# Optimization experiments

Hardware: AMD Instinct MI355X
Metric: run time of the kernel (lower is better)

Reference implementation:

```python
import jax, jax.numpy as jnp
import numpy as np

H = 256          # hidden_size
TH_X = 0.05      # delta threshold on inputs
TH_H = 0.05      # delta threshold on hidden state
F_IN = 6         # engineered feature count


def hardswish(v):
    return v * jnp.clip(v + 3.0, 0.0, 6.0) / 6.0


def setup_inputs() -> dict:
    key = jax.random.key(0)
    ks = jax.random.split(key, 6)
    B, T = 32, 4096
    x = jax.random.normal(ks[0], (B, T, 2), dtype=jnp.float32)
    # x2h: Linear(6, 3H, bias=False) -> weight (3H, 6)
    Wx = jax.random.normal(ks[1], (3 * H, F_IN), dtype=jnp.float32) * (1.0 / np.sqrt(F_IN))
    # h2h: Linear(H, 3H, bias=False) -> weight (3H, H)
    Wh = jax.random.normal(ks[2], (3 * H, H), dtype=jnp.float32) * (1.0 / np.sqrt(H))
    # fc_out: Linear(H, 2, bias=False)
    Wo = jax.random.normal(ks[3], (2, H), dtype=jnp.float32) * (1.0 / np.sqrt(H))
    # tcn conv1: Conv1d(2, 3, k=3, padding=16, dilation=16, bias=False) -> (O,I,K)=(3,2,3)
    Wc1 = jax.random.normal(ks[4], (3, 2, 3), dtype=jnp.float32) * 0.3
    # tcn conv2: Conv1d(3, 2, k=1) -> (2,3,1)
    Wc2 = jax.random.normal(ks[5], (2, 3, 1), dtype=jnp.float32) * 0.3
    return {"x": x, "Wx": Wx, "Wh": Wh, "Wo": Wo, "Wc1": Wc1, "Wc2": Wc2}


def _delta_gru(feats_TBF, Wx, Wh):
    # feats_TBF: (T, B, 6). Initial states are always zeros (the torch module
    # resets them whenever x_p_0 is None, which DeltaGRUModel always passes).
    T, B, F = feats_TBF.shape
    dt = feats_TBF.dtype
    carry0 = (
        jnp.zeros((B, F), dt),        # x_p
        jnp.zeros((B, H), dt),        # h
        jnp.zeros((B, H), dt),        # h_p
        jnp.zeros((B, H), dt),        # dm_nh
        jnp.zeros((B, 3 * H), dt),    # dm
    )

    def step(carry, xt):
        x_p, h, h_p, dm_nh, dm = carry
        dx = xt - x_p
        dh = h - h_p
        dxa = jnp.abs(dx)
        dha = jnp.abs(dh)
        dx = jnp.where(dxa < TH_X, 0.0, dx)
        dh = jnp.where(dha < TH_H, 0.0, dh)
        x_p = jnp.where(dxa >= TH_X, xt, x_p)
        h_p = jnp.where(dha >= TH_H, h, h_p)
        mac_x = dx @ Wx.T + dm          # (B, 3H)
        mac_h = dh @ Wh.T               # (B, 3H)
        mxr, mxz, mxn = jnp.split(mac_x, 3, axis=1)
        mhr, mhz, mhn = jnp.split(mac_h, 3, axis=1)
        dm_r = mxr + mhr
        dm_z = mxz + mhz
        dm_n = mxn
        dm_nh = mhn + dm_nh
        dm = jnp.concatenate([dm_r, dm_z, dm_n], axis=1)
        r = jax.nn.sigmoid(dm_r)
        z = jax.nn.sigmoid(dm_z)
        n = jnp.tanh(dm_n + r * dm_nh)
        h = (1.0 - z) * n + z * h
        return (x_p, h, h_p, dm_nh, dm), h

    _, hs = jax.lax.scan(step, carry0, feats_TBF)  # hs: (T, B, H)
    return hs


def reference(x, Wx, Wh, Wo, Wc1, Wc2):
    # x: (B, T, 2)
    B, T, _ = x.shape
    # --- TCN skip path ---
    xc = jnp.transpose(x, (0, 2, 1))  # (B, 2, T)
    c1 = jax.lax.conv_general_dilated(
        xc, Wc1, window_strides=(1,), padding=[(16, 16)], rhs_dilation=(16,),
        dimension_numbers=("NCH", "OIH", "NCH"))
    c2 = jax.lax.conv_general_dilated(
        hardswish(c1), Wc2, window_strides=(1,), padding=[(0, 0)],
        dimension_numbers=("NCH", "OIH", "NCH"))
    skip = jnp.transpose(hardswish(c2), (0, 2, 1))  # (B, T, 2)
    # --- engineered features ---
    i = x[..., 0:1]
    q = x[..., 1:2]
    amp2 = i * i + q * q
    amp = jnp.sqrt(jnp.maximum(amp2, 1e-12))
    amp3 = amp * amp2
    i_prev = jnp.pad(i[:, :-1, :], ((0, 0), (1, 0), (0, 0)))
    q_prev = jnp.pad(q[:, :-1, :], ((0, 0), (1, 0), (0, 0)))
    feats = jnp.concatenate([i, q, amp, amp3, i_prev, q_prev], axis=-1)  # (B,T,6)
    # --- delta-GRU scan (time-major) ---
    hs = _delta_gru(jnp.transpose(feats, (1, 0, 2)), Wx, Wh)  # (T, B, H)
    out = jnp.transpose(hs, (1, 0, 2))  # (B, T, H)
    return out @ Wo.T + skip  # (B, T, 2)
```

## Files before the change

### kernel.cpp

```cpp
#include <hip/hip_runtime.h>
#include <math.h>

#define HH 256
#define FIN 6
#define TT 4096
#define BB 32
#define TH 0.05f

typedef _Float16 h2 __attribute__((ext_vector_type(2)));
struct H8 { h2 a, b, c, d; };

__device__ __forceinline__ float hswish(float v) {
    float c = fminf(fmaxf(v + 3.0f, 0.0f), 6.0f);
    return v * c * (1.0f / 6.0f);
}
__device__ __forceinline__ float fexp2(float x) { return __builtin_amdgcn_exp2f(x); }
__device__ __forceinline__ float frcp(float x)  { return __builtin_amdgcn_rcpf(x); }
__device__ __forceinline__ float sigm(float x)  { return frcp(1.0f + fexp2(-1.44269504f * x)); }
__device__ __forceinline__ float tanhf_fast(float x) {
    float ax = fabsf(x);
    float e = fexp2(2.88539008f * ax);
    float t = 1.0f - 2.0f * frcp(e + 1.0f);
    return copysignf(t, x);
}

__device__ __forceinline__ float dpp_row_sum16(float p) {
    int x = __float_as_int(p);
    p += __int_as_float(__builtin_amdgcn_update_dpp(0, x, 0x118, 0xF, 0xF, true));
    x = __float_as_int(p);
    p += __int_as_float(__builtin_amdgcn_update_dpp(0, x, 0x114, 0xF, 0xF, true));
    x = __float_as_int(p);
    p += __int_as_float(__builtin_amdgcn_update_dpp(0, x, 0x112, 0xF, 0xF, true));
    x = __float_as_int(p);
    p += __int_as_float(__builtin_amdgcn_update_dpp(0, x, 0x111, 0xF, 0xF, true));
    return p;
}

__global__ __launch_bounds__(256) void k_prep(
        const float* __restrict__ x, const float* __restrict__ Wc1,
        const float* __restrict__ Wc2, float* __restrict__ feats,
        float* __restrict__ out) {
    int idx = blockIdx.x * 256 + threadIdx.x;
    if (idx >= BB * TT) return;
    int b = idx >> 12;
    int t = idx & (TT - 1);
    const float* xb = x + (size_t)b * TT * 2;
    float i0 = xb[t * 2 + 0], q0 = xb[t * 2 + 1];
    float ip = (t > 0) ? xb[(t - 1) * 2 + 0] : 0.0f;
    float qp = (t > 0) ? xb[(t - 1) * 2 + 1] : 0.0f;
    float amp2 = i0 * i0 + q0 * q0;
    float amp  = sqrtf(fmaxf(amp2, 1e-12f));
    float amp3 = amp * amp2;
    float* f = feats + (size_t)idx * 6;
    f[0] = i0; f[1] = q0; f[2] = amp; f[3] = amp3; f[4] = ip; f[5] = qp;

    float c1[3];
#pragma unroll
    for (int m = 0; m < 3; m++) {
        float acc = 0.0f;
#pragma unroll
        for (int k = 0; k < 3; k++) {
            int tt = t + (k - 1) * 16;
            if (tt >= 0 && tt < TT) {
                acc += Wc1[m * 6 + 0 * 3 + k] * xb[tt * 2 + 0];
                acc += Wc1[m * 6 + 1 * 3 + k] * xb[tt * 2 + 1];
            }
        }
        c1[m] = hswish(acc);
    }
#pragma unroll
    for (int o = 0; o < 2; o++) {
        float acc = Wc2[o * 3 + 0] * c1[0] + Wc2[o * 3 + 1] * c1[1] + Wc2[o * 3 + 2] * c1[2];
        out[(size_t)idx * 2 + o] = hswish(acc);
    }
}

__global__ __launch_bounds__(512)
__attribute__((amdgpu_waves_per_eu(2, 2))) void k_gru(
        const float* __restrict__ feats, const float* __restrict__ Wx,
        const float* __restrict__ Wh, const float* __restrict__ Wo,
        float* __restrict__ out) {
    __shared__ float s_out[TT * 2];
    __shared__ __align__(16) _Float16 s_dhh[2][HH];
    __shared__ __align__(16) float s_dx[2][8];
    __shared__ float s_feat[2][128 * FIN];

    const int tid  = threadIdx.x;
    const int wv   = tid >> 6;
    const int lane = tid & 63;
    const int half = lane >> 5;
    const int row  = wv * 32 + (lane & 31);
    const int b    = blockIdx.x;
    const float* fb = feats + (size_t)b * TT * FIN;

    for (int i = tid; i < TT * 2; i += 512) s_out[i] = 0.0f;
    for (int i = tid; i < 128 * FIN; i += 512) s_feat[0][i] = fb[i];

    h2 wr[64], wz[64], wn[64];
    {
        const int k0 = half * 128;
        const float4* p0 = (const float4*)(Wh + (size_t)(0 * HH + row) * HH + k0);
        const float4* p1 = (const float4*)(Wh + (size_t)(1 * HH + row) * HH + k0);
        const float4* p2 = (const float4*)(Wh + (size_t)(2 * HH + row) * HH + k0);
#pragma unroll
        for (int c = 0; c < 32; c++) {
            float4 v0 = p0[c], v1 = p1[c], v2 = p2[c];
            wr[2 * c]     = h2{(_Float16)v0.x, (_Float16)v0.y};
            wr[2 * c + 1] = h2{(_Float16)v0.z, (_Float16)v0.w};
            wz[2 * c]     = h2{(_Float16)v1.x, (_Float16)v1.y};
            wz[2 * c + 1] = h2{(_Float16)v1.z, (_Float16)v1.w};
            wn[2 * c]     = h2{(_Float16)v2.x, (_Float16)v2.y};
            wn[2 * c + 1] = h2{(_Float16)v2.z, (_Float16)v2.w};
        }
    }
    float wxr[FIN], wxz[FIN], wxn[FIN];
#pragma unroll
    for (int f = 0; f < FIN; f++) {
        wxr[f] = Wx[(size_t)(0 * HH + row) * FIN + f];
        wxz[f] = Wx[(size_t)(1 * HH + row) * FIN + f];
        wxn[f] = Wx[(size_t)(2 * HH + row) * FIN + f];
    }
    const float woc = Wo[half * HH + row];

    float h = 0.0f, hp = 0.0f, dmr = 0.0f, dmz = 0.0f, dmn = 0.0f, dmnh = 0.0f;
    float xp = 0.0f, curf = 0.0f;
    if (tid < FIN) curf = fb[tid];

    __syncthreads();

    for (int t = 0; t < TT; t++) {
        const int tb = t & 1;

        if ((t & 127) == 64 && t + 64 < TT) {
            const int w = (t >> 7) + 1;
            for (int i = tid; i < 128 * FIN; i += 512)
                s_feat[w & 1][i] = fb[(size_t)w * 128 * FIN + i];
        }

        {
            float dh = h - hp;
            bool keep = fabsf(dh) >= TH;
            if (half == 0) s_dhh[tb][row] = (_Float16)(keep ? dh : 0.0f);
            if (keep) hp = h;
        }
        if (tid < FIN) {
            float dx = curf - xp;
            bool keep = fabsf(dx) >= TH;
            s_dx[tb][tid] = keep ? dx : 0.0f;
            if (keep) xp = curf;
        }
        __syncthreads();

        float mxr = dmr, mxz = dmz, mxn = dmn;
        {
            const float4* dx4 = (const float4*)s_dx[tb];
            float4 da = dx4[0], db = dx4[1];
            mxr = fmaf(da.x, wxr[0], mxr); mxz = fmaf(da.x, wxz[0], mxz); mxn = fmaf(da.x, wxn[0], mxn);
            mxr = fmaf(da.y, wxr[1], mxr); mxz = fmaf(da.y, wxz[1], mxz); mxn = fmaf(da.y, wxn[1], mxn);
            mxr = fmaf(da.z, wxr[2], mxr); mxz = fmaf(da.z, wxz[2], mxz); mxn = fmaf(da.z, wxn[2], mxn);
            mxr = fmaf(da.w, wxr[3], mxr); mxz = fmaf(da.w, wxz[3], mxz); mxn = fmaf(da.w, wxn[3], mxn);
            mxr = fmaf(db.x, wxr[4], mxr); mxz = fmaf(db.x, wxz[4], mxz); mxn = fmaf(db.x, wxn[4], mxn);
            mxr = fmaf(db.y, wxr[5], mxr); mxz = fmaf(db.y, wxz[5], mxz); mxn = fmaf(db.y, wxn[5], mxn);
        }
        float ar0 = 0.0f, az0 = 0.0f, an0 = 0.0f;
        float ar1 = 0.0f, az1 = 0.0f, an1 = 0.0f;
        {
            const H8* dp = (const H8*)s_dhh[tb] + half * 16;
#pragma unroll
            for (int c = 0; c < 16; c += 2) {
                H8 d0 = dp[c];
                H8 d1 = dp[c + 1];
                ar0 = __builtin_amdgcn_fdot2(d0.a, wr[4 * c + 0], ar0, false);
                az0 = __builtin_amdgcn_fdot2(d0.a, wz[4 * c + 0], az0, false);
                an0 = __builtin_amdgcn_fdot2(d0.a, wn[4 * c + 0], an0, false);
                ar1 = __builtin_amdgcn_fdot2(d1.a, wr[4 * c + 4], ar1, false);
                az1 = __builtin_amdgcn_fdot2(d1.a, wz[4 * c + 4], az1, false);
                an1 = __builtin_amdgcn_fdot2(d1.a, wn[4 * c + 4], an1, false);
                ar0 = __builtin_amdgcn_fdot2(d0.b, wr[4 * c + 1], ar0, false);
                az0 = __builtin_amdgcn_fdot2(d0.b, wz[4 * c + 1], az0, false);
                an0 = __builtin_amdgcn_fdot2(d0.b, wn[4 * c + 1], an0, false);
                ar1 = __builtin_amdgcn_fdot2(d1.b, wr[4 * c + 5], ar1, false);
                az1 = __builtin_amdgcn_fdot2(d1.b, wz[4 * c + 5], az1, false);
                an1 = __builtin_amdgcn_fdot2(d1.b, wn[4 * c + 5], an1, false);
                ar0 = __builtin_amdgcn_fdot2(d0.c, wr[4 * c + 2], ar0, false);
                az0 = __builtin_amdgcn_fdot2(d0.c, wz[4 * c + 2], az0, false);
                an0 = __builtin_amdgcn_fdot2(d0.c, wn[4 * c + 2], an0, false);
                ar1 = __builtin_amdgcn_fdot2(d1.c, wr[4 * c + 6], ar1, false);
                az1 = __builtin_amdgcn_fdot2(d1.c, wz[4 * c + 6], az1, false);
                an1 = __builtin_amdgcn_fdot2(d1.c, wn[4 * c + 6], an1, false);
                ar0 = __builtin_amdgcn_fdot2(d0.d, wr[4 * c + 3], ar0, false);
                az0 = __builtin_amdgcn_fdot2(d0.d, wz[4 * c + 3], az0, false);
                an0 = __builtin_amdgcn_fdot2(d0.d, wn[4 * c + 3], an0, false);
                ar1 = __builtin_amdgcn_fdot2(d1.d, wr[4 * c + 7], ar1, false);
                az1 = __builtin_amdgcn_fdot2(d1.d, wz[4 * c + 7], az1, false);
                an1 = __builtin_amdgcn_fdot2(d1.d, wn[4 * c + 7], an1, false);
            }
        }
        float ar = ar0 + ar1, az = az0 + az1, an = an0 + an1;
        ar += __shfl_xor(ar, 32, 64);
        az += __shfl_xor(az, 32, 64);
        an += __shfl_xor(an, 32, 64);

        dmr = mxr + ar;
        dmz = mxz + az;
        dmn = mxn;
        dmnh += an;

        {
            float r = sigm(dmr);
            float z = sigm(dmz);
            float nn = tanhf_fast(dmn + r * dmnh);
            h = (1.0f - z) * nn + z * h;
        }

        {
            float p = h * woc;
            p += __shfl_xor(p, 16, 64);
            p = dpp_row_sum16(p);
            if ((lane & 31) == 31) atomicAdd(&s_out[2 * t + half], p);
        }

        if (tid < FIN && t + 1 < TT) {
            const int tn = t + 1;
            curf = s_feat[(tn >> 7) & 1][(tn & 127) * FIN + tid];
        }
    }

    __syncthreads();
    const size_t outbase = (size_t)b * TT * 2;
    for (int i = tid; i < TT * 2; i += 512) out[outbase + i] += s_out[i];
}

extern "C" void kernel_launch(void* const* d_in, const int* in_sizes, int n_in,
                              void* d_out, int out_size, void* d_ws, size_t ws_size,
                              hipStream_t stream) {
    const float* x   = (const float*)d_in[0];
    const float* Wx  = (const float*)d_in[1];
    const float* Wh  = (const float*)d_in[2];
    const float* Wo  = (const float*)d_in[3];
    const float* Wc1 = (const float*)d_in[4];
    const float* Wc2 = (const float*)d_in[5];
    float* out = (float*)d_out;
    float* feats = (float*)d_ws;

    k_prep<<<(BB * TT + 255) / 256, 256, 0, stream>>>(x, Wc1, Wc2, feats, out);
    k_gru<<<BB, 512, 0, stream>>>(feats, Wx, Wh, Wo, out);
}
```

Measured before the change: 4.995 ms.

## Broadcast hidden-delta slices across lanes via DPP instead of LDS loads

Each lane in a group of four now loads only a quarter of the fp16 hidden-delta vector from shared memory. DPP quad_perm broadcasts then give every lane each of the four slices in turn before the dot products. This cuts LDS read traffic and the latency of the wide shared loads on the serial recurrence path. In exchange it adds DPP moves, and it relies on the weight register layout matching the new lane-to-slice ordering.

```diff
diff --git a/kernel.cpp b/kernel.cpp
--- a/kernel.cpp
+++ b/kernel.cpp
@@ -162,40 +162,41 @@
             mxr = fmaf(db.x, wxr[4], mxr); mxz = fmaf(db.x, wxz[4], mxz); mxn = fmaf(db.x, wxn[4], mxn);
             mxr = fmaf(db.y, wxr[5], mxr); mxz = fmaf(db.y, wxz[5], mxz); mxn = fmaf(db.y, wxn[5], mxn);
         }
+
+        h2 dsl[16];
+        {
+            const H8* p8 = (const H8*)(s_dhh[tb] + half * 128 + (lane & 3) * 32);
+            H8 e0 = p8[0], e1 = p8[1], e2 = p8[2], e3 = p8[3];
+            dsl[0]  = e0.a; dsl[1]  = e0.b; dsl[2]  = e0.c; dsl[3]  = e0.d;
+            dsl[4]  = e1.a; dsl[5]  = e1.b; dsl[6]  = e1.c; dsl[7]  = e1.d;
+            dsl[8]  = e2.a; dsl[9]  = e2.b; dsl[10] = e2.c; dsl[11] = e2.d;
+            dsl[12] = e3.a; dsl[13] = e3.b; dsl[14] = e3.c; dsl[15] = e3.d;
+        }
         float ar0 = 0.0f, az0 = 0.0f, an0 = 0.0f;
         float ar1 = 0.0f, az1 = 0.0f, an1 = 0.0f;
-        {
-            const H8* dp = (const H8*)s_dhh[tb] + half * 16;
-#pragma unroll
-            for (int c = 0; c < 16; c += 2) {
-                H8 d0 = dp[c];
-                H8 d1 = dp[c + 1];
-                ar0 = __builtin_amdgcn_fdot2(d0.a, wr[4 * c + 0], ar0, false);
-                az0 = __builtin_amdgcn_fdot2(d0.a, wz[4 * c + 0], az0, false);
-                an0 = __builtin_amdgcn_fdot2(d0.a, wn[4 * c + 0], an0, false);
-                ar1 = __builtin_amdgcn_fdot2(d1.a, wr[4 * c + 4], ar1, false);
-                az1 = __builtin_amdgcn_fdot2(d1.a, wz[4 * c + 4], az1, false);
-                an1 = __builtin_amdgcn_fdot2(d1.a, wn[4 * c + 4], an1, false);
-                ar0 = __builtin_amdgcn_fdot2(d0.b, wr[4 * c + 1], ar0, false);
-                az0 = __builtin_amdgcn_fdot2(d0.b, wz[4 * c + 1], az0, false);
-                an0 = __builtin_amdgcn_fdot2(d0.b, wn[4 * c + 1], an0, false);
-                ar1 = __builtin_amdgcn_fdot2(d1.b, wr[4 * c + 5], ar1, false);
-                az1 = __builtin_amdgcn_fdot2(d1.b, wz[4 * c + 5], az1, false);
-                an1 = __builtin_amdgcn_fdot2(d1.b, wn[4 * c + 5], an1, false);
-                ar0 = __builtin_amdgcn_fdot2(d0.c, wr[4 * c + 2], ar0, false);
-                az0 = __builtin_amdgcn_fdot2(d0.c, wz[4 * c + 2], az0, false);
-                an0 = __builtin_amdgcn_fdot2(d0.c, wn[4 * c + 2], an0, false);
-                ar1 = __builtin_amdgcn_fdot2(d1.c, wr[4 * c + 6], ar1, false);
-                az1 = __builtin_amdgcn_fdot2(d1.c, wz[4 * c + 6], az1, false);
-                an1 = __builtin_amdgcn_fdot2(d1.c, wn[4 * c + 6], an1, false);
-                ar0 = __builtin_amdgcn_fdot2(d0.d, wr[4 * c + 3], ar0, false);
-                az0 = __builtin_amdgcn_fdot2(d0.d, wz[4 * c + 3], az0, false);
-                an0 = __builtin_amdgcn_fdot2(d0.d, wn[4 * c + 3], an0, false);
-                ar1 = __builtin_amdgcn_fdot2(d1.d, wr[4 * c + 7], ar1, false);
-                az1 = __builtin_amdgcn_fdot2(d1.d, wz[4 * c + 7], az1, false);
-                an1 = __builtin_amdgcn_fdot2(d1.d, wn[4 * c + 7], an1, false);
-            }
-        }
+#define GATE_DOTS(CTRL, P)                                                     \
+        {                                                                      \
+            _Pragma("unroll")                                                  \
+            for (int j = 0; j < 16; j += 2) {                                  \
+                int t0_ = __builtin_amdgcn_update_dpp(                         \
+                    0, __builtin_bit_cast(int, dsl[j]), (CTRL), 0xF, 0xF, true);\
+                int t1_ = __builtin_amdgcn_update_dpp(                         \
+                    0, __builtin_bit_cast(int, dsl[j + 1]), (CTRL), 0xF, 0xF, true);\
+                h2 s0_ = __builtin_bit_cast(h2, t0_);                          \
+                h2 s1_ = __builtin_bit_cast(h2, t1_);                          \
+                ar0 = __builtin_amdgcn_fdot2(s0_, wr[(P) * 16 + j], ar0, false);\
+                az0 = __builtin_amdgcn_fdot2(s0_, wz[(P) * 16 + j], az0, false);\
+                an0 = __builtin_amdgcn_fdot2(s0_, wn[(P) * 16 + j], an0, false);\
+                ar1 = __builtin_amdgcn_fdot2(s1_, wr[(P) * 16 + j + 1], ar1, false);\
+                az1 = __builtin_amdgcn_fdot2(s1_, wz[(P) * 16 + j + 1], az1, false);\
+                an1 = __builtin_amdgcn_fdot2(s1_, wn[(P) * 16 + j + 1], an1, false);\
+            }                                                                  \
+        }
+        GATE_DOTS(0x00, 0)
+        GATE_DOTS(0x55, 1)
+        GATE_DOTS(0xAA, 2)
+        GATE_DOTS(0xFF, 3)
+#undef GATE_DOTS
         float ar = ar0 + ar1, az = az0 + az1, an = an0 + an1;
         ar += __shfl_xor(ar, 32, 64);
         az += __shfl_xor(az, 32, 64);
```

Measured after the change: 5.690 ms. 1.14x slower.
